# Kernel optimization log

Measured on AMD Instinct MI355X. Metric: run time of the kernel, lower is better.

Reference implementation:

```python
import jax, jax.numpy as jnp
import numpy as np

B, LC, LQ, D, F = 16, 2048, 256, 768, 768
MASK_VALUE = -1.0e12


def setup_inputs() -> dict:
    key = jax.random.key(0)
    ks = jax.random.split(key, 6)
    scale = 1.0 / np.sqrt(D)
    return {
        "x_cont": jax.random.normal(ks[0], (B, LC, D), dtype=jnp.float32),
        "x_ques": jax.random.normal(ks[1], (B, LQ, D), dtype=jnp.float32),
        "ques_len": jax.random.randint(ks[2], (B, 1), 0, LQ, dtype=jnp.int32),
        "WC": jax.random.normal(ks[3], (D, F), dtype=jnp.float32) * scale,
        "WQ": jax.random.normal(ks[4], (D, F), dtype=jnp.float32) * scale,
        "V": jax.random.normal(ks[5], (2 * D, F), dtype=jnp.float32) * scale,
    }


def _mask_logits(logits, ques_len):
    # Original: one_hot(ques_len[:,0], Lq) -> 1 - cumsum along Lq -> tile over Lc.
    # mask[b, j] = 1 if j < ques_len[b] else 0.
    lq = logits.shape[-1]
    oh = jax.nn.one_hot(ques_len[:, 0], lq, dtype=jnp.float32)  # [B, Lq]
    valid = 1.0 - jnp.cumsum(oh, axis=1)                         # [B, Lq]
    return logits + MASK_VALUE * (1.0 - valid)[:, None, :]       # broadcast over Lc


def reference(x_cont, x_ques, ques_len, WC, WQ, V):
    filters = WC.shape[-1]
    x_cont_ = jax.nn.relu(jnp.einsum("bcd,df->bcf", x_cont, WC))  # [B, Lc, F]
    x_ques_ = jax.nn.relu(jnp.einsum("bqd,df->bqf", x_ques, WQ))  # [B, Lq, F]
    logits = jnp.einsum("bcf,bqf->bcq", x_cont_, x_ques_) / jnp.sqrt(
        jnp.asarray(filters, dtype=x_cont.dtype)
    )  # [B, Lc, Lq]
    logits = _mask_logits(logits, ques_len)
    attn = jax.nn.softmax(logits, axis=-1)
    C = jnp.einsum("bcq,bqd->bcd", attn, x_ques)                  # [B, Lc, D]
    res = jnp.concatenate([x_cont, C], axis=2)                    # [B, Lc, 2D]
    gate = jax.nn.sigmoid(jnp.einsum("bce,ef->bcf", res, V))      # [B, Lc, F]
    return gate
```

## Files before the change

kernel.cpp:

```cpp
#include <hip/hip_runtime.h>
#include <hip/hip_bf16.h>
#include <cstdint>


using bf16 = __hip_bfloat16;
typedef __attribute__((ext_vector_type(8))) __bf16 bf16x8;
typedef __attribute__((ext_vector_type(4))) float f32x4;

typedef __attribute__((address_space(1))) const uint32_t GU32;
typedef __attribute__((address_space(3))) uint32_t LU32;

__device__ __forceinline__ void gll16(const bf16* g, bf16* l) {
  __builtin_amdgcn_global_load_lds((GU32*)g, (LU32*)l, 16, 0, 0);
}
__device__ __forceinline__ f32x4 mfma_bf16(bf16x8 a, bf16x8 b, f32x4 c) {
  return __builtin_amdgcn_mfma_f32_16x16x32_bf16(a, b, c, 0, 0, 0);
}
__device__ __forceinline__ bf16x8 ld_frag(const bf16* p) {
  return *reinterpret_cast<const bf16x8*>(p);
}
__device__ __forceinline__ int swz(int r) { return (r & 3) ^ ((r >> 2) & 1); }

__device__ __forceinline__ unsigned short f2bf_bits(float x) {
  bf16 b = __float2bfloat16(x);
  union { bf16 b; unsigned short s; } u;
  u.b = b;
  return u.s;
}

__global__ void transpose_f32_bf16(const float* __restrict__ in, bf16* __restrict__ out,
                                   int R, int C) {
  __shared__ float tile[32][33];
  int c0 = blockIdx.x * 32, r0 = blockIdx.y * 32;
  int tx = threadIdx.x, ty = threadIdx.y;
#pragma unroll
  for (int i = ty; i < 32; i += 8)
    tile[i][tx] = in[(long)(r0 + i) * C + (c0 + tx)];
  __syncthreads();
#pragma unroll
  for (int i = ty; i < 32; i += 8)
    out[(long)(c0 + i) * R + (r0 + tx)] = __float2bfloat16(tile[tx][i]);
}

__global__ void transpose_bf16(const bf16* __restrict__ in, bf16* __restrict__ out,
                               int R, int C, long ibs, long obs) {
  __shared__ bf16 tile[32][33];
  const bf16* inb = in + (long)blockIdx.z * ibs;
  bf16* outb = out + (long)blockIdx.z * obs;
  int c0 = blockIdx.x * 32, r0 = blockIdx.y * 32;
  int tx = threadIdx.x, ty = threadIdx.y;
#pragma unroll
  for (int i = ty; i < 32; i += 8)
    tile[i][tx] = inb[(long)(r0 + i) * C + (c0 + tx)];
  __syncthreads();
#pragma unroll
  for (int i = ty; i < 32; i += 8)
    outb[(long)(c0 + i) * R + (r0 + tx)] = tile[tx][i];
}

__global__ void convert_flat(const float* __restrict__ in, bf16* __restrict__ out, long n4) {
  long i = (long)blockIdx.x * blockDim.x + threadIdx.x;
  if (i >= n4) return;
  float4 v = reinterpret_cast<const float4*>(in)[i];
  ushort4 o;
  o.x = f2bf_bits(v.x);
  o.y = f2bf_bits(v.y);
  o.z = f2bf_bits(v.z);
  o.w = f2bf_bits(v.w);
  reinterpret_cast<ushort4*>(out)[i] = o;
}

__global__ __launch_bounds__(256) void gemm_bt_split(
    const bf16* __restrict__ A, long lda,
    const bf16* __restrict__ Bt, long ldb,
    bf16* __restrict__ O1, bf16* __restrict__ O2, int K) {
  __shared__ __align__(16) bf16 As[128 * 32];
  __shared__ __align__(16) bf16 Bs[128 * 32];
  const int tid = threadIdx.x;
  const int wave = tid >> 6;
  const int lane = tid & 63;
  const int l16 = lane & 15;
  const int kh = lane >> 4;
  const int wm = (wave >> 1) * 64;
  const int wn = (wave & 1) * 64;
  const long row0 = (long)blockIdx.x * 128;
  const long col0 = (long)blockIdx.y * 128;
  const int srow = tid >> 2;
  const int scol = ((tid & 3) ^ swz(srow)) * 8;

  const bf16* ap0 = A + (row0 + srow) * lda + scol;
  const bf16* ap1 = ap0 + 64 * lda;
  const bf16* bp0 = Bt + (col0 + srow) * ldb + scol;
  const bf16* bp1 = bp0 + 64 * ldb;
  bf16* as0 = As + wave * 512;
  bf16* as1 = as0 + 2048;
  bf16* bs0 = Bs + wave * 512;
  bf16* bs1 = bs0 + 2048;

  const int xc = (kh ^ swz(l16)) * 8;
  f32x4 acc[4][4] = {};

  for (int k0 = 0; k0 < K; k0 += 32) {
    gll16(ap0 + k0, as0);
    gll16(ap1 + k0, as1);
    gll16(bp0 + k0, bs0);
    gll16(bp1 + k0, bs1);
    __syncthreads();
    bf16x8 af[4], bfr[4];
#pragma unroll
    for (int i = 0; i < 4; ++i)
      af[i] = ld_frag(As + (wm + i * 16 + l16) * 32 + xc);
#pragma unroll
    for (int j = 0; j < 4; ++j)
      bfr[j] = ld_frag(Bs + (wn + j * 16 + l16) * 32 + xc);
#pragma unroll
    for (int i = 0; i < 4; ++i)
#pragma unroll
      for (int j = 0; j < 4; ++j)
        acc[i][j] = mfma_bf16(af[i], bfr[j], acc[i][j]);
    __syncthreads();
  }

  const bool isO1 = col0 < 768;
#pragma unroll
  for (int i = 0; i < 4; ++i)
#pragma unroll
    for (int j = 0; j < 4; ++j)
#pragma unroll
      for (int r = 0; r < 4; ++r) {
        long row = row0 + wm + i * 16 + kh * 4 + r;
        long col = col0 + wn + j * 16 + l16;
        float v = acc[i][j][r];
        if (isO1)
          O1[row * 768 + col] = __float2bfloat16(fmaxf(v, 0.0f));
        else
          O2[row * 768 + (col - 768)] = __float2bfloat16(v);
      }
}

__global__ __launch_bounds__(512, 2) void gemm4b(
    const bf16* __restrict__ A, long lda,
    const bf16* __restrict__ Bt, long ldb,
    bf16* __restrict__ O1, bf16* __restrict__ O2, int K) {
  extern __shared__ __align__(16) bf16 smem[];
  const int tid = threadIdx.x;
  const int wid = tid >> 6;
  const int lane = tid & 63;
  const int l15 = lane & 15;
  const int g = lane >> 4;
  const int wm = wid >> 2;
  const int wn = wid & 3;

  const int lin = blockIdx.x;
  const int per = (int)gridDim.x >> 3;
  const int wgid = (lin & 7) * per + (lin >> 3);
  const long row0 = (long)(wgid / 6) * 256;
  const long col0 = (long)(wgid % 6) * 256;

  const int srow = lane >> 2;
  const int sc = ((lane & 3) ^ swz(srow)) * 8;
  const int w16 = wid * 16;
  const bf16* Ab = A + (row0 + srow) * lda + sc;
  const bf16* Bb = Bt + (col0 + srow) * ldb + sc;

  f32x4 acc[8][4] = {};

  auto stageA = [&](int buf, int kk) {
    bf16* d = smem + buf * 16384 + w16 * 32;
    gll16(Ab + (long)w16 * lda + kk, d);
    gll16(Ab + (long)(128 + w16) * lda + kk, d + 128 * 32);
  };
  auto stageB = [&](int buf, int kk) {
    bf16* d = smem + buf * 16384 + 8192 + w16 * 32;
    gll16(Bb + (long)w16 * ldb + kk, d);
    gll16(Bb + (long)(128 + w16) * ldb + kk, d + 128 * 32);
  };
  const int xc = (g ^ swz(l15)) * 8;
  auto ldA = [&](int buf, int m) {
    int row = wm * 128 + m * 16 + l15;
    return ld_frag(smem + buf * 16384 + row * 32 + xc);
  };
  auto ldB = [&](int buf, int n) {
    int row = wn * 64 + n * 16 + l15;
    return ld_frag(smem + buf * 16384 + 8192 + row * 32 + xc);
  };

  stageA(0, 0);
  stageB(0, 0);
  stageA(1, 32);
  stageB(1, 32);
  stageA(2, 64);
  stageB(2, 64);
  asm volatile("s_waitcnt vmcnt(8)\n\ts_barrier" ::: "memory");

  const int NT = K >> 5;
  bf16x8 av[4], bv[4];

  for (int t = 0; t < NT; ++t) {
    const int cur = t & 3;
    const int pfb = (t + 3) & 3;
    const bool pf = (t + 3) < NT;
    const int kk = (t + 3) << 5;

#pragma unroll
    for (int n = 0; n < 4; ++n) bv[n] = ldB(cur, n);
#pragma unroll
    for (int m = 0; m < 4; ++m) av[m] = ldA(cur, m);
    if (pf) stageA(pfb, kk);
    __builtin_amdgcn_s_barrier();
    __builtin_amdgcn_s_setprio(1);
#pragma unroll
    for (int m = 0; m < 4; ++m)
#pragma unroll
      for (int n = 0; n < 4; ++n) acc[m][n] = mfma_bf16(av[m], bv[n], acc[m][n]);
    __builtin_amdgcn_s_setprio(0);
    __builtin_amdgcn_s_barrier();

#pragma unroll
    for (int m = 0; m < 4; ++m) av[m] = ldA(cur, 4 + m);
    if (pf) stageB(pfb, kk);
    __builtin_amdgcn_s_barrier();
    __builtin_amdgcn_s_setprio(1);
#pragma unroll
    for (int m = 0; m < 4; ++m)
#pragma unroll
      for (int n = 0; n < 4; ++n)
        acc[4 + m][n] = mfma_bf16(av[m], bv[n], acc[4 + m][n]);
    __builtin_amdgcn_s_setprio(0);

    if (t <= NT - 4)
      asm volatile("s_waitcnt vmcnt(8)\n\ts_barrier" ::: "memory");
    else if (t == NT - 3)
      asm volatile("s_waitcnt vmcnt(4)\n\ts_barrier" ::: "memory");
    else if (t == NT - 2)
      asm volatile("s_waitcnt vmcnt(0)\n\ts_barrier" ::: "memory");
  }

  const bool isO1 = col0 < 768;
#pragma unroll
  for (int m = 0; m < 8; ++m)
#pragma unroll
    for (int n = 0; n < 4; ++n)
#pragma unroll
      for (int r = 0; r < 4; ++r) {
        long row = row0 + wm * 128 + m * 16 + g * 4 + r;
        long col = col0 + wn * 64 + n * 16 + l15;
        float v = acc[m][n][r];
        if (isO1)
          O1[row * 768 + col] = __float2bfloat16(fmaxf(v, 0.0f));
        else
          O2[row * 768 + (col - 768)] = __float2bfloat16(v);
      }
}

__global__ __launch_bounds__(512, 2) void attn_kernel(
    const bf16* __restrict__ xcW, const bf16* __restrict__ xqW,
    const bf16* __restrict__ xqVT, const bf16* __restrict__ G1,
    const int* __restrict__ qlen_arr, float* __restrict__ out) {
  extern __shared__ __align__(16) bf16 smem[];
  bf16* P = smem + 24576;
  float* wred = (float*)(smem + 58368);
  float* wsum = wred + 512;

  const int n = blockIdx.x;
  const int xcd = n & 7;
  const int idx = n >> 3;
  const int b = xcd * 2 + (idx >> 4);
  const int ct = idx & 15;

  const int tid = threadIdx.x;
  const int wid = tid >> 6;
  const int lane = tid & 63;
  const int l16 = lane & 15;
  const int kh = lane >> 4;
  const int wr = wid >> 2;
  const int wc = wid & 3;

  const long crow0 = (long)b * 2048 + (long)ct * 128;
  const int srow = lane >> 2;
  const int sc = ((lane & 3) ^ swz(srow)) * 8;
  const int xcr = (kh ^ swz(l16)) * 8;

  const bf16* ap = xcW + (crow0 + wid * 16 + srow) * 768 + sc;
  const bf16* bp = xqW + ((long)b * 256 + wid * 32 + srow) * 768 + sc;
  const bf16* bp2 = bp + 16 * 768;

  auto stage = [&](int bufi, int k0) {
    gll16(ap + k0, smem + bufi * 4096 + wid * 512);
    gll16(bp + k0, smem + 8192 + bufi * 8192 + wid * 1024);
    gll16(bp2 + k0, smem + 8192 + bufi * 8192 + wid * 1024 + 512);
  };

  f32x4 acc[4][4] = {};
  stage(0, 0);

  for (int t = 0; t < 24; ++t) {
    const int cur = t & 1;
    if (t + 1 < 24) {
      stage(cur ^ 1, (t + 1) * 32);
      asm volatile("s_waitcnt vmcnt(3)\n\ts_barrier" ::: "memory");
    } else {
      asm volatile("s_waitcnt vmcnt(0)\n\ts_barrier" ::: "memory");
    }
    const bf16* Ac = smem + cur * 4096;
    const bf16* Bc = smem + 8192 + cur * 8192;
    bf16x8 af[4], bfr[4];
#pragma unroll
    for (int i = 0; i < 4; ++i)
      af[i] = ld_frag(Ac + (wr * 64 + i * 16 + l16) * 32 + xcr);
#pragma unroll
    for (int j = 0; j < 4; ++j)
      bfr[j] = ld_frag(Bc + (wc * 64 + j * 16 + l16) * 32 + xcr);
    __builtin_amdgcn_s_setprio(1);
#pragma unroll
    for (int i = 0; i < 4; ++i)
#pragma unroll
      for (int j = 0; j < 4; ++j)
        acc[i][j] = mfma_bf16(af[i], bfr[j], acc[i][j]);
    __builtin_amdgcn_s_setprio(0);
    __builtin_amdgcn_s_barrier();
  }

  const float scale = 0.036084391824351615f;
  const int qlen = qlen_arr[b];

#pragma unroll
  for (int i = 0; i < 4; ++i)
#pragma unroll
    for (int j = 0; j < 4; ++j) {
      int col = wc * 64 + j * 16 + l16;
      float m = (col >= qlen) ? -1.0e12f : 0.0f;
#pragma unroll
      for (int r = 0; r < 4; ++r)
        acc[i][j][r] = acc[i][j][r] * scale + m;
    }

#pragma unroll
  for (int i = 0; i < 4; ++i)
#pragma unroll
    for (int r = 0; r < 4; ++r) {
      float mx = fmaxf(fmaxf(acc[i][0][r], acc[i][1][r]),
                       fmaxf(acc[i][2][r], acc[i][3][r]));
      mx = fmaxf(mx, __shfl_xor(mx, 1));
      mx = fmaxf(mx, __shfl_xor(mx, 2));
      mx = fmaxf(mx, __shfl_xor(mx, 4));
      mx = fmaxf(mx, __shfl_xor(mx, 8));
      if (l16 == 0) wred[(wr * 64 + i * 16 + kh * 4 + r) * 4 + wc] = mx;
    }
  __syncthreads();

#pragma unroll
  for (int i = 0; i < 4; ++i)
#pragma unroll
    for (int r = 0; r < 4; ++r) {
      int row = wr * 64 + i * 16 + kh * 4 + r;
      float gm = fmaxf(fmaxf(wred[row * 4 + 0], wred[row * 4 + 1]),
                       fmaxf(wred[row * 4 + 2], wred[row * 4 + 3]));
      float s = 0.0f;
#pragma unroll
      for (int j = 0; j < 4; ++j) {
        float e = expf(acc[i][j][r] - gm);
        acc[i][j][r] = e;
        s += e;
      }
      s += __shfl_xor(s, 1);
      s += __shfl_xor(s, 2);
      s += __shfl_xor(s, 4);
      s += __shfl_xor(s, 8);
      if (l16 == 0) wsum[row * 4 + wc] = s;
    }
  __syncthreads();

#pragma unroll
  for (int i = 0; i < 4; ++i)
#pragma unroll
    for (int r = 0; r < 4; ++r) {
      int row = wr * 64 + i * 16 + kh * 4 + r;
      float inv = 1.0f / (wsum[row * 4 + 0] + wsum[row * 4 + 1] +
                          wsum[row * 4 + 2] + wsum[row * 4 + 3]);
#pragma unroll
      for (int j = 0; j < 4; ++j)
        P[row * 264 + wc * 64 + j * 16 + l16] = __float2bfloat16(acc[i][j][r] * inv);
    }
  __syncthreads();

  bf16x8 pf[4][8];
#pragma unroll
  for (int i = 0; i < 4; ++i)
#pragma unroll
    for (int kk = 0; kk < 8; ++kk)
      pf[i][kk] = ld_frag(P + (wr * 64 + i * 16 + l16) * 264 + kk * 32 + kh * 8);

  for (int nb = 0; nb < 3; ++nb) {
    const int n0 = nb * 256 + wc * 64;
    const bf16* btp = xqVT + ((long)b * 768 + n0) * 256;
    f32x4 a2[4][4] = {};
#pragma unroll
    for (int kk = 0; kk < 8; ++kk) {
      bf16x8 vf[4];
#pragma unroll
      for (int j = 0; j < 4; ++j)
        vf[j] = ld_frag(btp + (j * 16 + l16) * 256 + kk * 32 + kh * 8);
#pragma unroll
      for (int i = 0; i < 4; ++i)
#pragma unroll
        for (int j = 0; j < 4; ++j)
          a2[i][j] = mfma_bf16(pf[i][kk], vf[j], a2[i][j]);
    }
#pragma unroll
    for (int i = 0; i < 4; ++i)
#pragma unroll
      for (int j = 0; j < 4; ++j)
#pragma unroll
        for (int r = 0; r < 4; ++r) {
          long row = crow0 + wr * 64 + i * 16 + kh * 4 + r;
          int col = n0 + j * 16 + l16;
          float v = a2[i][j][r] + __bfloat162float(G1[row * 768 + col]);
          out[row * 768 + col] = 1.0f / (1.0f + __expf(-v));
        }
  }
}

extern "C" void kernel_launch(void* const* d_in, const int* in_sizes, int n_in,
                              void* d_out, int out_size, void* d_ws, size_t ws_size,
                              hipStream_t stream) {
  const float* x_cont = (const float*)d_in[0];
  const float* x_ques = (const float*)d_in[1];
  const int* ques_len = (const int*)d_in[2];
  const float* WC = (const float*)d_in[3];
  const float* WQ = (const float*)d_in[4];
  const float* V = (const float*)d_in[5];
  float* out = (float*)d_out;

  bf16* Wct = (bf16*)d_ws;
  bf16* Wqt = Wct + (long)1536 * 768;
  bf16* xcB = Wqt + (long)1536 * 768;
  bf16* xqB = xcB + (long)32768 * 768;
  bf16* xcW = xqB + (long)4096 * 768;
  bf16* xqW = xcW + (long)32768 * 768;
  bf16* xqV = xqW + (long)4096 * 768;
  bf16* xqVT = xqV + (long)4096 * 768;
  bf16* G1 = xqVT + (long)16 * 768 * 256;

  (void)hipFuncSetAttribute(reinterpret_cast<const void*>(&gemm4b),
                            hipFuncAttributeMaxDynamicSharedMemorySize, 131072);
  (void)hipFuncSetAttribute(reinterpret_cast<const void*>(&attn_kernel),
                            hipFuncAttributeMaxDynamicSharedMemorySize, 131072);

  transpose_f32_bf16<<<dim3(24, 24), dim3(32, 8), 0, stream>>>(WC, Wct, 768, 768);
  transpose_f32_bf16<<<dim3(24, 24), dim3(32, 8), 0, stream>>>(
      V, Wct + (long)768 * 768, 768, 768);
  transpose_f32_bf16<<<dim3(24, 24), dim3(32, 8), 0, stream>>>(WQ, Wqt, 768, 768);
  transpose_f32_bf16<<<dim3(24, 24), dim3(32, 8), 0, stream>>>(
      V + (long)768 * 768, Wqt + (long)768 * 768, 768, 768);

  convert_flat<<<24576, 256, 0, stream>>>(x_cont, xcB, (long)32768 * 768 / 4);
  convert_flat<<<3072, 256, 0, stream>>>(x_ques, xqB, (long)4096 * 768 / 4);

  gemm_bt_split<<<dim3(32, 12), 256, 0, stream>>>(xqB, 768, Wqt, 768, xqW, xqV, 768);
  transpose_bf16<<<dim3(24, 8, 16), dim3(32, 8), 0, stream>>>(
      xqV, xqVT, 256, 768, (long)256 * 768, (long)768 * 256);

  gemm4b<<<768, 512, 131072, stream>>>(xcB, 768, Wct, 768, xcW, G1, 768);

  attn_kernel<<<256, 512, 120832, stream>>>(xcW, xqW, xqVT, G1, ques_len, out);
}
```

Baseline: 255.7 us.

## Fuse fp32-to-bf16 conversion of x_cont into GEMM and shrink attention tiles

```diff
diff --git a/kernel.cpp b/kernel.cpp
--- a/kernel.cpp
+++ b/kernel.cpp
@@ -27,19 +27,32 @@
   u.b = b;
   return u.s;
 }
-
-__global__ void transpose_f32_bf16(const float* __restrict__ in, bf16* __restrict__ out,
-                                   int R, int C) {
+__device__ __forceinline__ bf16x8 pack_bf16x8(f32x4 a, f32x4 b) {
+  union { bf16x8 v; bf16 e[8]; } u;
+#pragma unroll
+  for (int i = 0; i < 4; ++i) u.e[i] = __float2bfloat16(a[i]);
+#pragma unroll
+  for (int i = 0; i < 4; ++i) u.e[4 + i] = __float2bfloat16(b[i]);
+  return u.v;
+}
+
+__global__ void transpose4(const float* __restrict__ s0, const float* __restrict__ s1,
+                           const float* __restrict__ s2, const float* __restrict__ s3,
+                           bf16* __restrict__ d0, bf16* __restrict__ d1,
+                           bf16* __restrict__ d2, bf16* __restrict__ d3) {
   __shared__ float tile[32][33];
+  const int z = blockIdx.z;
+  const float* in = (z == 0) ? s0 : (z == 1) ? s1 : (z == 2) ? s2 : s3;
+  bf16* out = (z == 0) ? d0 : (z == 1) ? d1 : (z == 2) ? d2 : d3;
   int c0 = blockIdx.x * 32, r0 = blockIdx.y * 32;
   int tx = threadIdx.x, ty = threadIdx.y;
 #pragma unroll
   for (int i = ty; i < 32; i += 8)
-    tile[i][tx] = in[(long)(r0 + i) * C + (c0 + tx)];
+    tile[i][tx] = in[(long)(r0 + i) * 768 + (c0 + tx)];
   __syncthreads();
 #pragma unroll
   for (int i = ty; i < 32; i += 8)
-    out[(long)(c0 + i) * R + (r0 + tx)] = __float2bfloat16(tile[tx][i]);
+    out[(long)(c0 + i) * 768 + (r0 + tx)] = __float2bfloat16(tile[tx][i]);
 }
 
 __global__ void transpose_bf16(const bf16* __restrict__ in, bf16* __restrict__ out,
@@ -138,10 +151,9 @@
       }
 }
 
-__global__ __launch_bounds__(512, 2) void gemm4b(
-    const bf16* __restrict__ A, long lda,
-    const bf16* __restrict__ Bt, long ldb,
-    bf16* __restrict__ O1, bf16* __restrict__ O2, int K) {
+__global__ __launch_bounds__(512) void gemm4b(
+    const float* __restrict__ Af, const bf16* __restrict__ Bt,
+    bf16* __restrict__ O1, bf16* __restrict__ O2) {
   extern __shared__ __align__(16) bf16 smem[];
   const int tid = threadIdx.x;
   const int wid = tid >> 6;
@@ -152,28 +164,37 @@
   const int wn = wid & 3;
 
   const int lin = blockIdx.x;
-  const int per = (int)gridDim.x >> 3;
-  const int wgid = (lin & 7) * per + (lin >> 3);
+  const int xcd = lin & 7;
+  const int jj = lin >> 3;
+  const int wgid = xcd * 96 + jj;
   const long row0 = (long)(wgid / 6) * 256;
   const long col0 = (long)(wgid % 6) * 256;
+
+  const int arow = tid >> 1;
+  const int ahalf = tid & 1;
+  const float* Ap = Af + (row0 + arow) * 768 + ahalf * 16;
+  const int awz = swz(arow & 15);
 
   const int srow = lane >> 2;
   const int sc = ((lane & 3) ^ swz(srow)) * 8;
   const int w16 = wid * 16;
-  const bf16* Ab = A + (row0 + srow) * lda + sc;
-  const bf16* Bb = Bt + (col0 + srow) * ldb + sc;
+  const bf16* Bb = Bt + (col0 + srow) * 768 + sc;
 
   f32x4 acc[8][4] = {};
 
-  auto stageA = [&](int buf, int kk) {
-    bf16* d = smem + buf * 16384 + w16 * 32;
-    gll16(Ab + (long)w16 * lda + kk, d);
-    gll16(Ab + (long)(128 + w16) * lda + kk, d + 128 * 32);
-  };
   auto stageB = [&](int buf, int kk) {
     bf16* d = smem + buf * 16384 + 8192 + w16 * 32;
-    gll16(Bb + (long)w16 * ldb + kk, d);
-    gll16(Bb + (long)(128 + w16) * ldb + kk, d + 128 * 32);
+    gll16(Bb + (long)w16 * 768 + kk, d);
+    gll16(Bb + (long)(128 + w16) * 768 + kk, d + 128 * 32);
+  };
+  auto writeA = [&](int buf, const f32x4* ar) {
+    bf16* base = smem + buf * 16384 + arow * 32;
+#pragma unroll
+    for (int q = 0; q < 2; ++q) {
+      int c = ahalf * 2 + q;
+      *reinterpret_cast<bf16x8*>(base + ((c ^ awz) * 8)) =
+          pack_bf16x8(ar[2 * q], ar[2 * q + 1]);
+    }
   };
   const int xc = (g ^ swz(l15)) * 8;
   auto ldA = [&](int buf, int m) {
@@ -185,55 +206,49 @@
     return ld_frag(smem + buf * 16384 + 8192 + row * 32 + xc);
   };
 
-  stageA(0, 0);
+  f32x4 ar[4];
+#pragma unroll
+  for (int q = 0; q < 4; ++q) ar[q] = *reinterpret_cast<const f32x4*>(Ap + q * 4);
   stageB(0, 0);
-  stageA(1, 32);
   stageB(1, 32);
-  stageA(2, 64);
-  stageB(2, 64);
-  asm volatile("s_waitcnt vmcnt(8)\n\ts_barrier" ::: "memory");
-
-  const int NT = K >> 5;
-  bf16x8 av[4], bv[4];
-
-  for (int t = 0; t < NT; ++t) {
-    const int cur = t & 3;
-    const int pfb = (t + 3) & 3;
-    const bool pf = (t + 3) < NT;
-    const int kk = (t + 3) << 5;
-
+  asm volatile("s_waitcnt vmcnt(4)" ::: "memory");
+  writeA(0, ar);
+  asm volatile("s_waitcnt vmcnt(2) lgkmcnt(0)\n\ts_barrier" ::: "memory");
+
+  for (int t = 0; t < 24; ++t) {
+    const int cur = t % 3;
+    const int nxtb = (t + 1) % 3;
+    const int pf2b = (t + 2) % 3;
+
+    bf16x8 av[8], bv[4];
 #pragma unroll
     for (int n = 0; n < 4; ++n) bv[n] = ldB(cur, n);
 #pragma unroll
-    for (int m = 0; m < 4; ++m) av[m] = ldA(cur, m);
-    if (pf) stageA(pfb, kk);
-    __builtin_amdgcn_s_barrier();
+    for (int m = 0; m < 8; ++m) av[m] = ldA(cur, m);
+    if (t + 1 < 24) {
+      const float* ap = Ap + (t + 1) * 32;
+#pragma unroll
+      for (int q = 0; q < 4; ++q) ar[q] = *reinterpret_cast<const f32x4*>(ap + q * 4);
+    }
+    if (t + 2 < 24) stageB(pf2b, (t + 2) * 32);
+    __builtin_amdgcn_sched_barrier(0);
+
     __builtin_amdgcn_s_setprio(1);
 #pragma unroll
-    for (int m = 0; m < 4; ++m)
-#pragma unroll
-      for (int n = 0; n < 4; ++n) acc[m][n] = mfma_bf16(av[m], bv[n], acc[m][n]);
+    for (int m = 0; m < 8; ++m)
+#pragma unroll
+      for (int n = 0; n < 4; ++n)
+        acc[m][n] = mfma_bf16(av[m], bv[n], acc[m][n]);
     __builtin_amdgcn_s_setprio(0);
-    __builtin_amdgcn_s_barrier();
-
-#pragma unroll
-    for (int m = 0; m < 4; ++m) av[m] = ldA(cur, 4 + m);
-    if (pf) stageB(pfb, kk);
-    __builtin_amdgcn_s_barrier();
-    __builtin_amdgcn_s_setprio(1);
-#pragma unroll
-    for (int m = 0; m < 4; ++m)
-#pragma unroll
-      for (int n = 0; n < 4; ++n)
-        acc[4 + m][n] = mfma_bf16(av[m], bv[n], acc[4 + m][n]);
-    __builtin_amdgcn_s_setprio(0);
-
-    if (t <= NT - 4)
-      asm volatile("s_waitcnt vmcnt(8)\n\ts_barrier" ::: "memory");
-    else if (t == NT - 3)
-      asm volatile("s_waitcnt vmcnt(4)\n\ts_barrier" ::: "memory");
-    else if (t == NT - 2)
-      asm volatile("s_waitcnt vmcnt(0)\n\ts_barrier" ::: "memory");
+
+    if (t + 1 < 24) {
+      if (t + 2 < 24)
+        asm volatile("s_waitcnt vmcnt(2)" ::: "memory");
+      else
+        asm volatile("s_waitcnt vmcnt(0)" ::: "memory");
+      writeA(nxtb, ar);
+      asm volatile("s_waitcnt lgkmcnt(0)\n\ts_barrier" ::: "memory");
+    }
   }
 
   const bool isO1 = col0 < 768;
@@ -253,42 +268,41 @@
       }
 }
 
-__global__ __launch_bounds__(512, 2) void attn_kernel(
+__global__ __launch_bounds__(256) void attn_kernel(
     const bf16* __restrict__ xcW, const bf16* __restrict__ xqW,
     const bf16* __restrict__ xqVT, const bf16* __restrict__ G1,
     const int* __restrict__ qlen_arr, float* __restrict__ out) {
   extern __shared__ __align__(16) bf16 smem[];
-  bf16* P = smem + 24576;
-  float* wred = (float*)(smem + 58368);
-  float* wsum = wred + 512;
+  bf16* P = smem + 20480;
+  float* wred = (float*)(smem + 37376);
+  float* wsum = wred + 256;
 
   const int n = blockIdx.x;
   const int xcd = n & 7;
   const int idx = n >> 3;
-  const int b = xcd * 2 + (idx >> 4);
-  const int ct = idx & 15;
+  const int b = xcd * 2 + (idx >> 5);
+  const int ct = idx & 31;
 
   const int tid = threadIdx.x;
-  const int wid = tid >> 6;
+  const int wc = tid >> 6;
   const int lane = tid & 63;
   const int l16 = lane & 15;
   const int kh = lane >> 4;
-  const int wr = wid >> 2;
-  const int wc = wid & 3;
-
-  const long crow0 = (long)b * 2048 + (long)ct * 128;
+
+  const long crow0 = (long)b * 2048 + (long)ct * 64;
   const int srow = lane >> 2;
   const int sc = ((lane & 3) ^ swz(srow)) * 8;
   const int xcr = (kh ^ swz(l16)) * 8;
 
-  const bf16* ap = xcW + (crow0 + wid * 16 + srow) * 768 + sc;
-  const bf16* bp = xqW + ((long)b * 256 + wid * 32 + srow) * 768 + sc;
-  const bf16* bp2 = bp + 16 * 768;
+  const bf16* ap = xcW + (crow0 + wc * 16 + srow) * 768 + sc;
+  const bf16* bp = xqW + ((long)b * 256 + wc * 64 + srow) * 768 + sc;
 
   auto stage = [&](int bufi, int k0) {
-    gll16(ap + k0, smem + bufi * 4096 + wid * 512);
-    gll16(bp + k0, smem + 8192 + bufi * 8192 + wid * 1024);
-    gll16(bp2 + k0, smem + 8192 + bufi * 8192 + wid * 1024 + 512);
+    gll16(ap + k0, smem + bufi * 2048 + wc * 512);
+    bf16* bd = smem + 4096 + bufi * 8192 + wc * 2048;
+#pragma unroll
+    for (int q = 0; q < 4; ++q)
+      gll16(bp + q * 16 * 768 + k0, bd + q * 512);
   };
 
   f32x4 acc[4][4] = {};
@@ -298,16 +312,16 @@
     const int cur = t & 1;
     if (t + 1 < 24) {
       stage(cur ^ 1, (t + 1) * 32);
-      asm volatile("s_waitcnt vmcnt(3)\n\ts_barrier" ::: "memory");
+      asm volatile("s_waitcnt vmcnt(5)\n\ts_barrier" ::: "memory");
     } else {
       asm volatile("s_waitcnt vmcnt(0)\n\ts_barrier" ::: "memory");
     }
-    const bf16* Ac = smem + cur * 4096;
-    const bf16* Bc = smem + 8192 + cur * 8192;
+    const bf16* Ac = smem + cur * 2048;
+    const bf16* Bc = smem + 4096 + cur * 8192;
     bf16x8 af[4], bfr[4];
 #pragma unroll
     for (int i = 0; i < 4; ++i)
-      af[i] = ld_frag(Ac + (wr * 64 + i * 16 + l16) * 32 + xcr);
+      af[i] = ld_frag(Ac + (i * 16 + l16) * 32 + xcr);
 #pragma unroll
     for (int j = 0; j < 4; ++j)
       bfr[j] = ld_frag(Bc + (wc * 64 + j * 16 + l16) * 32 + xcr);
@@ -345,7 +359,7 @@
       mx = fmaxf(mx, __shfl_xor(mx, 2));
       mx = fmaxf(mx, __shfl_xor(mx, 4));
       mx = fmaxf(mx, __shfl_xor(mx, 8));
-      if (l16 == 0) wred[(wr * 64 + i * 16 + kh * 4 + r) * 4 + wc] = mx;
+      if (l16 == 0) wred[(i * 16 + kh * 4 + r) * 4 + wc] = mx;
     }
   __syncthreads();
 
@@ -353,7 +367,7 @@
   for (int i = 0; i < 4; ++i)
 #pragma unroll
     for (int r = 0; r < 4; ++r) {
-      int row = wr * 64 + i * 16 + kh * 4 + r;
+      int row = i * 16 + kh * 4 + r;
       float gm = fmaxf(fmaxf(wred[row * 4 + 0], wred[row * 4 + 1]),
                        fmaxf(wred[row * 4 + 2], wred[row * 4 + 3]));
       float s = 0.0f;
@@ -375,7 +389,7 @@
   for (int i = 0; i < 4; ++i)
 #pragma unroll
     for (int r = 0; r < 4; ++r) {
-      int row = wr * 64 + i * 16 + kh * 4 + r;
+      int row = i * 16 + kh * 4 + r;
       float inv = 1.0f / (wsum[row * 4 + 0] + wsum[row * 4 + 1] +
                           wsum[row * 4 + 2] + wsum[row * 4 + 3]);
 #pragma unroll
@@ -389,7 +403,7 @@
   for (int i = 0; i < 4; ++i)
 #pragma unroll
     for (int kk = 0; kk < 8; ++kk)
-      pf[i][kk] = ld_frag(P + (wr * 64 + i * 16 + l16) * 264 + kk * 32 + kh * 8);
+      pf[i][kk] = ld_frag(P + (i * 16 + l16) * 264 + kk * 32 + kh * 8);
 
   for (int nb = 0; nb < 3; ++nb) {
     const int n0 = nb * 256 + wc * 64;
@@ -413,7 +427,7 @@
       for (int j = 0; j < 4; ++j)
 #pragma unroll
         for (int r = 0; r < 4; ++r) {
-          long row = crow0 + wr * 64 + i * 16 + kh * 4 + r;
+          long row = crow0 + i * 16 + kh * 4 + r;
           int col = n0 + j * 16 + l16;
           float v = a2[i][j][r] + __bfloat162float(G1[row * 768 + col]);
           out[row * 768 + col] = 1.0f / (1.0f + __expf(-v));
@@ -434,8 +448,7 @@
 
   bf16* Wct = (bf16*)d_ws;
   bf16* Wqt = Wct + (long)1536 * 768;
-  bf16* xcB = Wqt + (long)1536 * 768;
-  bf16* xqB = xcB + (long)32768 * 768;
+  bf16* xqB = Wqt + (long)1536 * 768;
   bf16* xcW = xqB + (long)4096 * 768;
   bf16* xqW = xcW + (long)32768 * 768;
   bf16* xqV = xqW + (long)4096 * 768;
@@ -443,25 +456,20 @@
   bf16* G1 = xqVT + (long)16 * 768 * 256;
 
   (void)hipFuncSetAttribute(reinterpret_cast<const void*>(&gemm4b),
-                            hipFuncAttributeMaxDynamicSharedMemorySize, 131072);
+                            hipFuncAttributeMaxDynamicSharedMemorySize, 98304);
   (void)hipFuncSetAttribute(reinterpret_cast<const void*>(&attn_kernel),
-                            hipFuncAttributeMaxDynamicSharedMemorySize, 131072);
-
-  transpose_f32_bf16<<<dim3(24, 24), dim3(32, 8), 0, stream>>>(WC, Wct, 768, 768);
-  transpose_f32_bf16<<<dim3(24, 24), dim3(32, 8), 0, stream>>>(
-      V, Wct + (long)768 * 768, 768, 768);
-  transpose_f32_bf16<<<dim3(24, 24), dim3(32, 8), 0, stream>>>(WQ, Wqt, 768, 768);
-  transpose_f32_bf16<<<dim3(24, 24), dim3(32, 8), 0, stream>>>(
-      V + (long)768 * 768, Wqt + (long)768 * 768, 768, 768);
-
-  convert_flat<<<24576, 256, 0, stream>>>(x_cont, xcB, (long)32768 * 768 / 4);
+                            hipFuncAttributeMaxDynamicSharedMemorySize, 76800);
+
+  transpose4<<<dim3(24, 24, 4), dim3(32, 8), 0, stream>>>(
+      WC, WQ, V, V + (long)768 * 768,
+      Wct, Wqt, Wct + (long)768 * 768, Wqt + (long)768 * 768);
+
   convert_flat<<<3072, 256, 0, stream>>>(x_ques, xqB, (long)4096 * 768 / 4);
-
   gemm_bt_split<<<dim3(32, 12), 256, 0, stream>>>(xqB, 768, Wqt, 768, xqW, xqV, 768);
   transpose_bf16<<<dim3(24, 8, 16), dim3(32, 8), 0, stream>>>(
       xqV, xqVT, 256, 768, (long)256 * 768, (long)768 * 256);
 
-  gemm4b<<<768, 512, 131072, stream>>>(xcB, 768, Wct, 768, xcW, G1, 768);
-
-  attn_kernel<<<256, 512, 120832, stream>>>(xcW, xqW, xqVT, G1, ques_len, out);
-}
+  gemm4b<<<768, 512, 98304, stream>>>(x_cont, Wct, xcW, G1);
+
+  attn_kernel<<<512, 256, 76800, stream>>>(xcW, xqW, xqVT, G1, ques_len, out);
+}
```

Measured after the change: 305.3 us. 1.19x slower.
